# Optimization experiments

Hardware: AMD Instinct MI355X
Metric: run time of the kernel (lower is better)

The kernel has to match this reference:

```python
import jax, jax.numpy as jnp
import numpy as np

RADIUS = 0.2
NSAMPLE = 32
NPOINT = 2048
EPS = 1e-5


def setup_inputs() -> dict:
    key = jax.random.key(0)
    ks = jax.random.split(key, 6)
    B, N, C = 8, 8192, 64
    xyz = jax.random.uniform(ks[0], (B, N, 3), dtype=jnp.float32)
    features = jax.random.normal(ks[1], (B, C, N), dtype=jnp.float32)
    W1 = jax.random.normal(ks[2], (64, 67), dtype=jnp.float32) * 0.1
    W2 = jax.random.normal(ks[3], (64, 64), dtype=jnp.float32) * 0.1
    W3 = jax.random.normal(ks[4], (128, 64), dtype=jnp.float32) * 0.1
    return {
        'xyz': xyz, 'features': features,
        'W1': W1, 'g1': jnp.ones((64,), jnp.float32), 'b1': jnp.zeros((64,), jnp.float32),
        'W2': W2, 'g2': jnp.ones((64,), jnp.float32), 'b2': jnp.zeros((64,), jnp.float32),
        'W3': W3, 'g3': jnp.ones((128,), jnp.float32), 'b3': jnp.zeros((128,), jnp.float32),
    }


def furthest_point_sample(xyz, npoint):
    # xyz: (B, N, 3) -> (B, npoint) int32 indices, first index is 0 (CUDA FPS convention)
    B, N, _ = xyz.shape
    idxs0 = jnp.zeros((B, npoint), dtype=jnp.int32)
    dists0 = jnp.full((B, N), 1e10, dtype=xyz.dtype)
    last0 = jnp.zeros((B,), dtype=jnp.int32)

    def body(i, state):
        idxs, dists, last = state
        last_pt = xyz[jnp.arange(B), last]                      # (B, 3)
        d = jnp.sum((xyz - last_pt[:, None, :]) ** 2, axis=-1)  # (B, N)
        dists = jnp.minimum(dists, d)
        nxt = jnp.argmax(dists, axis=-1).astype(jnp.int32)
        idxs = idxs.at[:, i].set(nxt)
        return (idxs, dists, nxt)

    idxs, _, _ = jax.lax.fori_loop(1, npoint, body, (idxs0, dists0, last0))
    return idxs


def ball_query(xyz, new_xyz, radius, nsample):
    # Returns (B, S, nsample) int32: first `nsample` points within radius of each
    # query center, padded with the first in-ball index (pointnet2 convention).
    N = xyz.shape[1]
    d2 = jnp.sum((new_xyz[:, :, None, :] - xyz[:, None, :, :]) ** 2, axis=-1)  # (B,S,N)
    key = jnp.where(d2 < radius * radius, jnp.arange(N, dtype=jnp.int32), N)
    neg_vals, _ = jax.lax.top_k(-key, nsample)   # k smallest keys = earliest in-ball indices
    cand = -neg_vals                             # (B, S, nsample)
    first = cand[..., :1]
    return jnp.where(cand < N, cand, first)


def reference(xyz, features, W1, g1, b1, W2, g2, b2, W3, g3, b3):
    B = xyz.shape[0]
    fps_idx = furthest_point_sample(xyz, NPOINT)              # (B, S)
    new_xyz = xyz[jnp.arange(B)[:, None], fps_idx]            # (B, S, 3)

    idx = ball_query(xyz, new_xyz, RADIUS, NSAMPLE)           # (B, S, ns)
    bb = jnp.arange(B)[:, None, None]
    grouped_xyz = xyz[bb, idx] - new_xyz[:, :, None, :]       # (B, S, ns, 3) relative coords
    grouped_f = features.transpose(0, 2, 1)[bb, idx]          # (B, S, ns, C)
    g = jnp.concatenate([grouped_xyz, grouped_f], axis=-1)    # (B, S, ns, 3+C)
    g = g.transpose(0, 3, 1, 2)                               # (B, 3+C, S, ns)

    for W, ga, be in ((W1, g1, b1), (W2, g2, b2), (W3, g3, b3)):
        h = jnp.einsum('oc,bcsn->bosn', W, g)                 # 1x1 conv
        mu = h.mean(axis=(0, 2, 3), keepdims=True)            # training-mode BN stats
        var = h.var(axis=(0, 2, 3), keepdims=True)
        h = (h - mu) / jnp.sqrt(var + EPS)
        g = jax.nn.relu(h * ga[None, :, None, None] + be[None, :, None, None])

    feats = g.max(axis=-1)                                    # (B, mlp[-1], S)
    return new_xyz, feats
```

## Files before the change

kernel.cpp:

```cpp
#include <hip/hip_runtime.h>
#include <hip/hip_bf16.h>
#include <stdint.h>

#define NB 8
#define NN 8192
#define NC 64
#define NS 2048
#define NK 32
#define NCOL (NB*NS*NK)

typedef float v2f __attribute__((ext_vector_type(2)));

__device__ __forceinline__ unsigned short f2bf(float x) {
    union { float f; unsigned u; } c; c.f = x;
    unsigned r = c.u + 0x7fffu + ((c.u >> 16) & 1u);
    return (unsigned short)(r >> 16);
}
__device__ __forceinline__ float bf2f(unsigned v16) {
    union { float f; unsigned u; } c; c.u = v16 << 16;
    return c.f;
}

template<int CTRL>
__device__ __forceinline__ unsigned long long dpp_max_u64(unsigned long long key) {
    int olo = __builtin_amdgcn_update_dpp(0, (int)(unsigned)key,        CTRL, 0xf, 0xf, true);
    int ohi = __builtin_amdgcn_update_dpp(0, (int)(unsigned)(key >> 32), CTRL, 0xf, 0xf, true);
    unsigned long long ok = ((unsigned long long)(unsigned)ohi << 32) | (unsigned)olo;
    return ok > key ? ok : key;
}
template<int CTRL>
__device__ __forceinline__ float dpp_add_f32(float x) {
    int o = __builtin_amdgcn_update_dpp(0, __float_as_int(x), CTRL, 0xf, 0xf, true);
    return x + __int_as_float(o);
}
template<int CTRL>
__device__ __forceinline__ float dpp_max_f32(float x) {
    int o = __builtin_amdgcn_update_dpp(__float_as_int(x), __float_as_int(x), CTRL, 0xf, 0xf, false);
    return fmaxf(x, __int_as_float(o));
}
template<int CTRL>
__device__ __forceinline__ float dpp_min_f32(float x) {
    int o = __builtin_amdgcn_update_dpp(__float_as_int(x), __float_as_int(x), CTRL, 0xf, 0xf, false);
    return fminf(x, __int_as_float(o));
}
template<int CTRL, int RM>
__device__ __forceinline__ unsigned dpp_add_u32(unsigned x) {
    int o = __builtin_amdgcn_update_dpp(0, (int)x, CTRL, RM, 0xf, true);
    return x + (unsigned)o;
}
__device__ __forceinline__ float wave_red_min(float x) {
    x = dpp_min_f32<0x111>(x); x = dpp_min_f32<0x112>(x);
    x = dpp_min_f32<0x114>(x); x = dpp_min_f32<0x118>(x);
    x = dpp_min_f32<0x142>(x); x = dpp_min_f32<0x143>(x);
    return __int_as_float(__builtin_amdgcn_readlane(__float_as_int(x), 63));
}
__device__ __forceinline__ float wave_red_max(float x) {
    x = dpp_max_f32<0x111>(x); x = dpp_max_f32<0x112>(x);
    x = dpp_max_f32<0x114>(x); x = dpp_max_f32<0x118>(x);
    x = dpp_max_f32<0x142>(x); x = dpp_max_f32<0x143>(x);
    return __int_as_float(__builtin_amdgcn_readlane(__float_as_int(x), 63));
}
__device__ __forceinline__ v2f relu2(v2f v) {
    v.x = fmaxf(v.x, 0.f); v.y = fmaxf(v.y, 0.f); return v;
}

__device__ __forceinline__ unsigned expand_bits10(unsigned v) {
    v = (v * 0x00010001u) & 0xFF0000FFu;
    v = (v * 0x00000101u) & 0x0F00F00Fu;
    v = (v * 0x00000011u) & 0xC30C30C3u;
    v = (v * 0x00000005u) & 0x49249249u;
    return v;
}
__global__ __launch_bounds__(1024) void sort_kernel(const float* __restrict__ xyz,
    float4* __restrict__ sorted)
{
    __shared__ unsigned cnt[2048];
    __shared__ unsigned codes[NN];
    __shared__ unsigned wsum[16];
    const int b = blockIdx.x;
    const int tid = threadIdx.x;
    const int w = tid >> 6;
    const int lane = tid & 63;
    const float* xb = xyz + (size_t)b * NN * 3;
    cnt[tid] = 0; cnt[tid + 1024] = 0;
    __syncthreads();
    for (int p = tid; p < NN; p += 1024) {
        float x = xb[3*p+0], y = xb[3*p+1], z = xb[3*p+2];
        int qx = (int)(x * 1024.f); qx = qx < 0 ? 0 : (qx > 1023 ? 1023 : qx);
        int qy = (int)(y * 1024.f); qy = qy < 0 ? 0 : (qy > 1023 ? 1023 : qy);
        int qz = (int)(z * 1024.f); qz = qz < 0 ? 0 : (qz > 1023 ? 1023 : qz);
        unsigned m = expand_bits10((unsigned)qx)
                   | (expand_bits10((unsigned)qy) << 1)
                   | (expand_bits10((unsigned)qz) << 2);
        unsigned bk = m >> 19;
        codes[p] = bk;
        atomicAdd(&cnt[bk], 1u);
    }
    __syncthreads();
    unsigned c0 = cnt[2*tid], c1 = cnt[2*tid+1];
    unsigned s = c0 + c1;
    unsigned v = s;
    v = dpp_add_u32<0x111, 0xf>(v);
    v = dpp_add_u32<0x112, 0xf>(v);
    v = dpp_add_u32<0x114, 0xf>(v);
    v = dpp_add_u32<0x118, 0xf>(v);
    v = dpp_add_u32<0x142, 0xa>(v);
    v = dpp_add_u32<0x143, 0xc>(v);
    if (lane == 63) wsum[w] = v;
    __syncthreads();
    unsigned wbase = 0;
#pragma unroll
    for (int j = 0; j < 15; ++j) {
        unsigned t = wsum[j];
        wbase += (j < w) ? t : 0u;
    }
    unsigned excl = wbase + v - s;
    cnt[2*tid]   = excl;
    cnt[2*tid+1] = excl + c0;
    __syncthreads();
    for (int p = tid; p < NN; p += 1024) {
        unsigned bk = codes[p];
        unsigned pos = atomicAdd(&cnt[bk], 1u);
        float4 o;
        o.x = xb[3*p+0]; o.y = xb[3*p+1]; o.z = xb[3*p+2];
        o.w = __int_as_float(p);
        sorted[(size_t)b * NN + pos] = o;
    }
}

__global__ __launch_bounds__(1024) void fps_kernel(const float* __restrict__ xyz,
    const float4* __restrict__ sorted,
    float* __restrict__ new_xyz, float* __restrict__ out_newxyz)
{
#pragma clang fp contract(off)
    const int b = blockIdx.x;
    const int tid = threadIdx.x;
    const int w = tid >> 6;
    const int lane = tid & 63;
    __shared__ float sx[NN], sy[NN], sz[NN];
    __shared__ float s_hist[NS * 3];
    __shared__ unsigned long long s_slot[3];
    const float4* sp = sorted + (size_t)b * NN + (size_t)w * 512 + lane;
    v2f px[4], py[4], pz[4], dmin[4];
    unsigned plo[8];
    float bnx = 1e30f, bny = 1e30f, bnz = 1e30f;
    float bxx = -1e30f, bxy = -1e30f, bxz = -1e30f;
#pragma unroll
    for (int m = 0; m < 4; ++m) {
        float4 a = sp[128*m];
        float4 c = sp[128*m + 64];
        px[m].x = a.x; px[m].y = c.x;
        py[m].x = a.y; py[m].y = c.y;
        pz[m].x = a.z; pz[m].y = c.z;
        dmin[m].x = 1e10f; dmin[m].y = 1e10f;
        int ia = __float_as_int(a.w), ic = __float_as_int(c.w);
        plo[2*m]   = ~(unsigned)ia;
        plo[2*m+1] = ~(unsigned)ic;
        sx[ia] = a.x; sy[ia] = a.y; sz[ia] = a.z;
        sx[ic] = c.x; sy[ic] = c.y; sz[ic] = c.z;
        bnx = fminf(bnx, fminf(a.x, c.x)); bxx = fmaxf(bxx, fmaxf(a.x, c.x));
        bny = fminf(bny, fminf(a.y, c.y)); bxy = fmaxf(bxy, fmaxf(a.y, c.y));
        bnz = fminf(bnz, fminf(a.z, c.z)); bxz = fmaxf(bxz, fmaxf(a.z, c.z));
    }
    bnx = wave_red_min(bnx); bny = wave_red_min(bny); bnz = wave_red_min(bnz);
    bxx = wave_red_max(bxx); bxy = wave_red_max(bxy); bxz = wave_red_max(bxz);

    const float* xb = xyz + (size_t)b * NN * 3;
    float lx = xb[0], ly = xb[1], lz = xb[2];
    if (tid == 0) {
        s_hist[0] = lx; s_hist[1] = ly; s_hist[2] = lz;
        s_slot[0] = 0ull; s_slot[1] = 0ull; s_slot[2] = 0ull;
    }
    float ckv = 1e30f;
    unsigned cklo = 0u;
    __syncthreads();

    int cur = 1, nxt = 2;
    for (int i = 1; i < NS; ++i) {
        if (tid == 0) s_slot[nxt] = 0ull;
        float cdx = fmaxf(fmaxf(bnx - lx, lx - bxx), 0.f);
        float cdy = fmaxf(fmaxf(bny - ly, ly - bxy), 0.f);
        float cdz = fmaxf(fmaxf(bnz - lz, lz - bxz), 0.f);
        float lb = (cdx*cdx + cdy*cdy) + cdz*cdz;
        if (!(lb >= ckv)) {
            v2f l2x; l2x.x = lx; l2x.y = lx;
            v2f l2y; l2y.x = ly; l2y.y = ly;
            v2f l2z; l2z.x = lz; l2z.y = lz;
            unsigned long long best = 0ull;
#pragma unroll
            for (int m = 0; m < 4; ++m) {
                v2f dx = px[m] - l2x;
                v2f dy = py[m] - l2y;
                v2f dz = pz[m] - l2z;
                v2f d = (dx*dx + dy*dy) + dz*dz;
                v2f dm;
                dm.x = fminf(dmin[m].x, d.x);
                dm.y = fminf(dmin[m].y, d.y);
                dmin[m] = dm;
                unsigned long long k0 =
                    ((unsigned long long)__float_as_uint(dm.x) << 32) | plo[2*m];
                unsigned long long k1 =
                    ((unsigned long long)__float_as_uint(dm.y) << 32) | plo[2*m+1];
                if (k0 > best) best = k0;
                if (k1 > best) best = k1;
            }
            best = dpp_max_u64<0x111>(best);
            best = dpp_max_u64<0x112>(best);
            best = dpp_max_u64<0x114>(best);
            best = dpp_max_u64<0x118>(best);
            best = dpp_max_u64<0x142>(best);
            best = dpp_max_u64<0x143>(best);
            ckv  = __uint_as_float((unsigned)__builtin_amdgcn_readlane((int)(best >> 32), 63));
            cklo = (unsigned)__builtin_amdgcn_readlane((int)(best & 0xffffffffull), 63);
        }
        if (lane == 0)
            atomicMax(&s_slot[cur],
                      ((unsigned long long)__float_as_uint(ckv) << 32) | cklo);
        __syncthreads();
        const unsigned long long k = s_slot[cur];
        const int ix = ~(int)(unsigned)(k & 0xffffffffull);
        lx = sx[ix]; ly = sy[ix]; lz = sz[ix];
        if (tid == 0) {
            s_hist[3*i+0] = lx; s_hist[3*i+1] = ly; s_hist[3*i+2] = lz;
        }
        cur = nxt;
        nxt = nxt + 1; if (nxt == 3) nxt = 0;
    }
    __syncthreads();
    float* nw = new_xyz + (size_t)b * NS * 3;
    float* ow = out_newxyz + (size_t)b * NS * 3;
    for (int t = tid; t < NS * 3; t += 1024) {
        float v = s_hist[t];
        nw[t] = v; ow[t] = v;
    }
}

__global__ __launch_bounds__(256) void transpose_kernel(const float* __restrict__ f,
    float* __restrict__ ft)
{
    __shared__ float tile[64][65];
    int b = blockIdx.y;
    int p0 = blockIdx.x * 64;
    for (int k = threadIdx.x; k < 64*64; k += 256) {
        int c = k >> 6, p = k & 63;
        tile[c][p] = f[((size_t)b * NC + c) * NN + p0 + p];
    }
    __syncthreads();
    for (int k = threadIdx.x; k < 64*64; k += 256) {
        int p = k >> 6, c = k & 63;
        ft[((size_t)b * NN + p0 + p) * NC + c] = tile[c][p];
    }
}

__global__ __launch_bounds__(256) void ballquery_kernel(const float* __restrict__ xyz,
    const float* __restrict__ new_xyz, int* __restrict__ idx)
{
#pragma clang fp contract(off)
    const int q = blockIdx.x * 4 + (threadIdx.x >> 6);
    const int lane = threadIdx.x & 63;
    const int b = q >> 11;
    const float r2 = (float)(0.2 * 0.2);
    const float* xb = xyz + (size_t)b * NN * 3;
    const float* nx = new_xyz + (size_t)q * 3;
    float qx = nx[0], qy = nx[1], qz = nx[2];
    int cnt = 0, first = -1;
    int* out = idx + (size_t)q * NK;
    for (int base = 0; base < NN; base += 64) {
        int p = base + lane;
        float x = xb[p*3+0], y = xb[p*3+1], z = xb[p*3+2];
        float dx = qx - x, dy = qy - y, dz = qz - z;
        float d2 = (dx*dx + dy*dy) + dz*dz;
        bool in = d2 < r2;
        unsigned long long m = __ballot(in);
        if (m) {
            if (first < 0) first = base + __builtin_ctzll(m);
            if (in) {
                int rank = cnt + __popcll(m & ((1ull << lane) - 1ull));
                if (rank < NK) out[rank] = p;
            }
            cnt += __popcll(m);
            if (cnt >= NK) break;
        }
    }
    for (int k = cnt + lane; k < NK; k += 64) out[k] = first;
}

__global__ __launch_bounds__(256, 2) void layer1_kernel(const float* __restrict__ xyz,
    const float* __restrict__ new_xyz, const int* __restrict__ idx,
    const float* __restrict__ ft, const float* __restrict__ W1,
    unsigned short* __restrict__ h1)
{
    const int col = blockIdx.x * 256 + threadIdx.x;
    const int b = col >> 16;
    const int s = (col >> 5) & 2047;
    const int p = idx[col];
    v2f g[34];
    float* gf = (float*)g;
    {
        const float* nx = new_xyz + ((size_t)(b * NS + s)) * 3;
        const float* xp = xyz + ((size_t)(b * NN + p)) * 3;
        gf[0] = xp[0] - nx[0]; gf[1] = xp[1] - nx[1]; gf[2] = xp[2] - nx[2];
    }
    const float4* fp = (const float4*)(ft + ((size_t)(b * NN + p)) * NC);
#pragma unroll
    for (int c4 = 0; c4 < 16; ++c4) {
        float4 v = fp[c4];
        gf[3 + 4*c4 + 0] = v.x; gf[3 + 4*c4 + 1] = v.y;
        gf[3 + 4*c4 + 2] = v.z; gf[3 + 4*c4 + 3] = v.w;
    }
    gf[67] = 0.f;
    uint4* dst = (uint4*)(h1 + (size_t)col * 64);
#pragma unroll
    for (int half = 0; half < 2; ++half) {
        float h[32];
#pragma unroll 4
        for (int o16 = 0; o16 < 32; ++o16) {
            const float* w = W1 + (half*32 + o16) * 67;
            v2f acc; acc.x = 0.f; acc.y = 0.f;
#pragma unroll
            for (int k = 0; k < 33; ++k) {
                v2f wv; wv.x = w[2*k]; wv.y = w[2*k+1];
                acc = wv * g[k] + acc;
            }
            h[o16] = fmaf(w[66], gf[66], acc.x + acc.y);
        }
#pragma unroll
        for (int k = 0; k < 4; ++k) {
            uint4 v;
            v.x = (unsigned)f2bf(h[8*k+0]) | ((unsigned)f2bf(h[8*k+1]) << 16);
            v.y = (unsigned)f2bf(h[8*k+2]) | ((unsigned)f2bf(h[8*k+3]) << 16);
            v.z = (unsigned)f2bf(h[8*k+4]) | ((unsigned)f2bf(h[8*k+5]) << 16);
            v.w = (unsigned)f2bf(h[8*k+6]) | ((unsigned)f2bf(h[8*k+7]) << 16);
            dst[half*4 + k] = v;
        }
    }
}

__global__ __launch_bounds__(256) void stats_kernel(const unsigned short* __restrict__ h,
    float* __restrict__ sums)
{
    __shared__ float ls[64], lq[64];
    const int tid = threadIdx.x;
    if (tid < 64) { ls[tid] = 0.f; lq[tid] = 0.f; }
    __syncthreads();
    float s[8] = {0,0,0,0,0,0,0,0}, q[8] = {0,0,0,0,0,0,0,0};
    const int gt = blockIdx.x * 256 + tid;
    const int G = gridDim.x * 256;
    const uint4* src = (const uint4*)h;
    const int nvec = NCOL * 8;
    for (int i = gt; i < nvec; i += G) {
        uint4 v = src[i];
        float f0 = bf2f(v.x & 0xffffu), f1 = bf2f(v.x >> 16);
        float f2 = bf2f(v.y & 0xffffu), f3 = bf2f(v.y >> 16);
        float f4 = bf2f(v.z & 0xffffu), f5 = bf2f(v.z >> 16);
        float f6 = bf2f(v.w & 0xffffu), f7 = bf2f(v.w >> 16);
        s[0] += f0; q[0] = fmaf(f0, f0, q[0]);
        s[1] += f1; q[1] = fmaf(f1, f1, q[1]);
        s[2] += f2; q[2] = fmaf(f2, f2, q[2]);
        s[3] += f3; q[3] = fmaf(f3, f3, q[3]);
        s[4] += f4; q[4] = fmaf(f4, f4, q[4]);
        s[5] += f5; q[5] = fmaf(f5, f5, q[5]);
        s[6] += f6; q[6] = fmaf(f6, f6, q[6]);
        s[7] += f7; q[7] = fmaf(f7, f7, q[7]);
    }
    const int obase = (tid & 7) * 8;
#pragma unroll
    for (int j = 0; j < 8; ++j) {
        atomicAdd(&ls[obase + j], s[j]);
        atomicAdd(&lq[obase + j], q[j]);
    }
    __syncthreads();
    if (tid < 64) {
        atomicAdd(&sums[tid*2+0], ls[tid]);
        atomicAdd(&sums[tid*2+1], lq[tid]);
    }
}

__global__ void finalize_kernel(const float* __restrict__ sums,
    const float* __restrict__ gamma, const float* __restrict__ beta,
    float* __restrict__ ab, int nch)
{
    int c = threadIdx.x;
    if (c < nch) {
        const float invM = 1.0f / 524288.0f;
        float mu = sums[c*2] * invM;
        float var = sums[c*2+1] * invM - mu * mu;
        float a = gamma[c] / sqrtf(var + 1e-5f);
        ab[c] = a;
        ab[nch + c] = fmaf(-mu, a, beta[c]);
    }
}

__global__ __launch_bounds__(256, 2) void layer2_kernel(const unsigned short* __restrict__ h1,
    const float* __restrict__ ab1, const float* __restrict__ W2,
    unsigned short* __restrict__ h2)
{
    const int col = blockIdx.x * 256 + threadIdx.x;
    const uint4* src = (const uint4*)(h1 + (size_t)col * 64);
    v2f g[32];
    float* gf = (float*)g;
#pragma unroll
    for (int k = 0; k < 8; ++k) {
        uint4 v = src[k];
        gf[8*k+0] = bf2f(v.x & 0xffffu); gf[8*k+1] = bf2f(v.x >> 16);
        gf[8*k+2] = bf2f(v.y & 0xffffu); gf[8*k+3] = bf2f(v.y >> 16);
        gf[8*k+4] = bf2f(v.z & 0xffffu); gf[8*k+5] = bf2f(v.z >> 16);
        gf[8*k+6] = bf2f(v.w & 0xffffu); gf[8*k+7] = bf2f(v.w >> 16);
    }
    const v2f* a2 = (const v2f*)ab1;
    const v2f* b2 = (const v2f*)(ab1 + 64);
#pragma unroll
    for (int k = 0; k < 32; ++k)
        g[k] = relu2(a2[k] * g[k] + b2[k]);
    uint4* dst = (uint4*)(h2 + (size_t)col * 64);
#pragma unroll
    for (int half = 0; half < 2; ++half) {
        float h[32];
#pragma unroll 4
        for (int o16 = 0; o16 < 32; ++o16) {
            const float* w = W2 + ((half*32 + o16) << 6);
            v2f acc; acc.x = 0.f; acc.y = 0.f;
#pragma unroll
            for (int k = 0; k < 32; ++k) {
                v2f wv; wv.x = w[2*k]; wv.y = w[2*k+1];
                acc = wv * g[k] + acc;
            }
            h[o16] = acc.x + acc.y;
        }
#pragma unroll
        for (int k = 0; k < 4; ++k) {
            uint4 v;
            v.x = (unsigned)f2bf(h[8*k+0]) | ((unsigned)f2bf(h[8*k+1]) << 16);
            v.y = (unsigned)f2bf(h[8*k+2]) | ((unsigned)f2bf(h[8*k+3]) << 16);
            v.z = (unsigned)f2bf(h[8*k+4]) | ((unsigned)f2bf(h[8*k+5]) << 16);
            v.w = (unsigned)f2bf(h[8*k+6]) | ((unsigned)f2bf(h[8*k+7]) << 16);
            dst[half*4 + k] = v;
        }
    }
}

__global__ __launch_bounds__(256, 2) void layer3_kernel(const unsigned short* __restrict__ h2,
    const float* __restrict__ ab2, const float* __restrict__ W3,
    float* __restrict__ hmax, float* __restrict__ hmin, float* __restrict__ sums3)
{
    __shared__ float ls[128], lq[128];
    const int tid = threadIdx.x;
    if (tid < 128) { ls[tid] = 0.f; lq[tid] = 0.f; }
    __syncthreads();
    const int col = blockIdx.x * 256 + tid;
    const int q = col >> 5;
    const uint4* src = (const uint4*)(h2 + (size_t)col * 64);
    v2f g[32];
    float* gf = (float*)g;
#pragma unroll
    for (int k = 0; k < 8; ++k) {
        uint4 v = src[k];
        gf[8*k+0] = bf2f(v.x & 0xffffu); gf[8*k+1] = bf2f(v.x >> 16);
        gf[8*k+2] = bf2f(v.y & 0xffffu); gf[8*k+3] = bf2f(v.y >> 16);
        gf[8*k+4] = bf2f(v.z & 0xffffu); gf[8*k+5] = bf2f(v.z >> 16);
        gf[8*k+6] = bf2f(v.w & 0xffffu); gf[8*k+7] = bf2f(v.w >> 16);
    }
    const v2f* a2 = (const v2f*)ab2;
    const v2f* b2 = (const v2f*)(ab2 + 64);
#pragma unroll
    for (int k = 0; k < 32; ++k)
        g[k] = relu2(a2[k] * g[k] + b2[k]);
    const bool leader = ((tid & 31) == 31);
#pragma unroll 2
    for (int o = 0; o < 128; ++o) {
        const float* w = W3 + (o << 6);
        v2f acc; acc.x = 0.f; acc.y = 0.f;
#pragma unroll
        for (int k = 0; k < 32; ++k) {
            v2f wv; wv.x = w[2*k]; wv.y = w[2*k+1];
            acc = wv * g[k] + acc;
        }
        float hv = acc.x + acc.y;
        float sm = hv, sq = hv*hv, mx = hv, mn = hv;
        sm = dpp_add_f32<0x111>(sm); sq = dpp_add_f32<0x111>(sq);
        mx = dpp_max_f32<0x111>(mx); mn = dpp_min_f32<0x111>(mn);
        sm = dpp_add_f32<0x112>(sm); sq = dpp_add_f32<0x112>(sq);
        mx = dpp_max_f32<0x112>(mx); mn = dpp_min_f32<0x112>(mn);
        sm = dpp_add_f32<0x114>(sm); sq = dpp_add_f32<0x114>(sq);
        mx = dpp_max_f32<0x114>(mx); mn = dpp_min_f32<0x114>(mn);
        sm = dpp_add_f32<0x118>(sm); sq = dpp_add_f32<0x118>(sq);
        mx = dpp_max_f32<0x118>(mx); mn = dpp_min_f32<0x118>(mn);
        sm = dpp_add_f32<0x142>(sm); sq = dpp_add_f32<0x142>(sq);
        mx = dpp_max_f32<0x142>(mx); mn = dpp_min_f32<0x142>(mn);
        if (leader) {
            hmax[(size_t)o * 16384 + q] = mx;
            hmin[(size_t)o * 16384 + q] = mn;
            atomicAdd(&ls[o], sm);
            atomicAdd(&lq[o], sq);
        }
    }
    __syncthreads();
    if (tid < 128) {
        atomicAdd(&sums3[tid*2+0], ls[tid]);
        atomicAdd(&sums3[tid*2+1], lq[tid]);
    }
}

__global__ __launch_bounds__(256) void final_kernel(const float* __restrict__ hmax,
    const float* __restrict__ hmin, const float* __restrict__ ab3,
    float* __restrict__ out)
{
    const int t = blockIdx.x * 256 + threadIdx.x;
    const int s = t & 2047;
    const int o = (t >> 11) & 127;
    const int b = t >> 18;
    const int q = (b << 11) + s;
    float a = ab3[o], c = ab3[128 + o];
    float h = (a >= 0.f) ? hmax[(size_t)o * 16384 + q] : hmin[(size_t)o * 16384 + q];
    out[t] = fmaxf(fmaf(a, h, c), 0.f);
}

extern "C" void kernel_launch(void* const* d_in, const int* in_sizes, int n_in,
                              void* d_out, int out_size, void* d_ws, size_t ws_size,
                              hipStream_t stream) {
    (void)in_sizes; (void)n_in; (void)out_size; (void)ws_size;
    const float* xyz      = (const float*)d_in[0];
    const float* features = (const float*)d_in[1];
    const float* W1 = (const float*)d_in[2];
    const float* g1 = (const float*)d_in[3];
    const float* b1 = (const float*)d_in[4];
    const float* W2 = (const float*)d_in[5];
    const float* g2 = (const float*)d_in[6];
    const float* b2 = (const float*)d_in[7];
    const float* W3 = (const float*)d_in[8];
    const float* g3 = (const float*)d_in[9];
    const float* b3 = (const float*)d_in[10];

    char* ws = (char*)d_ws;
    float*          new_xyz = (float*)(ws + 0);
    int*            idx     = (int*)(ws + 196608);
    float*          ft      = (float*)(ws + 2293760);
    unsigned short* h1      = (unsigned short*)(ws + 19070976);
    unsigned short* h2      = (unsigned short*)(ws + 86179840);
    float*          hmax    = (float*)(ws + 153288704);
    float*          hmin    = (float*)(ws + 161677312);
    float*          sums    = (float*)(ws + 170065920);
    float*          ab      = (float*)(ws + 170067968);
    float* sums1 = sums;        float* ab1 = ab;
    float* sums2 = sums + 128;  float* ab2 = ab + 128;
    float* sums3 = sums + 256;  float* ab3 = ab + 256;

    float4* sorted = (float4*)h1;

    float* out_newxyz = (float*)d_out;
    float* out_feats  = (float*)d_out + 49152;

    hipMemsetAsync(sums, 0, 2048, stream);

    sort_kernel<<<NB, 1024, 0, stream>>>(xyz, sorted);
    fps_kernel<<<NB, 1024, 0, stream>>>(xyz, sorted, new_xyz, out_newxyz);
    transpose_kernel<<<dim3(NN/64, NB), 256, 0, stream>>>(features, ft);
    ballquery_kernel<<<(NB*NS)/4, 256, 0, stream>>>(xyz, new_xyz, idx);
    layer1_kernel<<<NCOL/256, 256, 0, stream>>>(xyz, new_xyz, idx, ft, W1, h1);
    stats_kernel<<<1024, 256, 0, stream>>>(h1, sums1);
    finalize_kernel<<<1, 128, 0, stream>>>(sums1, g1, b1, ab1, 64);
    layer2_kernel<<<NCOL/256, 256, 0, stream>>>(h1, ab1, W2, h2);
    stats_kernel<<<1024, 256, 0, stream>>>(h2, sums2);
    finalize_kernel<<<1, 128, 0, stream>>>(sums2, g2, b2, ab2, 64);
    layer3_kernel<<<NCOL/256, 256, 0, stream>>>(h2, ab2, W3, hmax, hmin, sums3);
    finalize_kernel<<<1, 128, 0, stream>>>(sums3, g3, b3, ab3, 128);
    final_kernel<<<(NB*128*NS)/256, 256, 0, stream>>>(hmax, hmin, ab3, out_feats);
}
```

Baseline: 2.039 ms.

## Use bf16 MFMA for layer-3 conv and simplify FPS atomic key

Rewrites the layer-3 1x1 convolution to use 16x16x32 bf16 MFMA instructions instead of per-thread scalar FMAs. Each wave now handles two 32-sample groups, applies the BN2 affine and ReLU while packing activations into bf16 fragments, and keeps per-channel sums and sums of squares in registers, reducing them once at the end. Max and min are reduced with DPP across the 16 columns. The weights are now rounded to bf16, which lowers precision, and W3 is re-converted on every tile. In FPS, lane 63 submits the full 64-bit key directly, dropping one readlane per iteration.

```diff
diff --git a/kernel.cpp b/kernel.cpp
--- a/kernel.cpp
+++ b/kernel.cpp
@@ -10,6 +10,8 @@
 #define NCOL (NB*NS*NK)
 
 typedef float v2f __attribute__((ext_vector_type(2)));
+typedef __attribute__((ext_vector_type(8))) short bf16x8;
+typedef __attribute__((ext_vector_type(4))) float f32x4;
 
 __device__ __forceinline__ unsigned short f2bf(float x) {
     union { float f; unsigned u; } c; c.f = x;
@@ -172,7 +174,7 @@
         s_slot[0] = 0ull; s_slot[1] = 0ull; s_slot[2] = 0ull;
     }
     float ckv = 1e30f;
-    unsigned cklo = 0u;
+    unsigned long long kc = 0ull;
     __syncthreads();
 
     int cur = 1, nxt = 2;
@@ -210,12 +212,11 @@
             best = dpp_max_u64<0x118>(best);
             best = dpp_max_u64<0x142>(best);
             best = dpp_max_u64<0x143>(best);
-            ckv  = __uint_as_float((unsigned)__builtin_amdgcn_readlane((int)(best >> 32), 63));
-            cklo = (unsigned)__builtin_amdgcn_readlane((int)(best & 0xffffffffull), 63);
-        }
-        if (lane == 0)
-            atomicMax(&s_slot[cur],
-                      ((unsigned long long)__float_as_uint(ckv) << 32) | cklo);
+            kc = best;
+            ckv = __uint_as_float((unsigned)__builtin_amdgcn_readlane((int)(best >> 32), 63));
+        }
+        if (lane == 63)
+            atomicMax(&s_slot[cur], kc);
         __syncthreads();
         const unsigned long long k = s_slot[cur];
         const int ix = ~(int)(unsigned)(k & 0xffffffffull);
@@ -447,49 +448,86 @@
     const int tid = threadIdx.x;
     if (tid < 128) { ls[tid] = 0.f; lq[tid] = 0.f; }
     __syncthreads();
-    const int col = blockIdx.x * 256 + tid;
-    const int q = col >> 5;
-    const uint4* src = (const uint4*)(h2 + (size_t)col * 64);
-    v2f g[32];
-    float* gf = (float*)g;
-#pragma unroll
-    for (int k = 0; k < 8; ++k) {
-        uint4 v = src[k];
-        gf[8*k+0] = bf2f(v.x & 0xffffu); gf[8*k+1] = bf2f(v.x >> 16);
-        gf[8*k+2] = bf2f(v.y & 0xffffu); gf[8*k+3] = bf2f(v.y >> 16);
-        gf[8*k+4] = bf2f(v.z & 0xffffu); gf[8*k+5] = bf2f(v.z >> 16);
-        gf[8*k+6] = bf2f(v.w & 0xffffu); gf[8*k+7] = bf2f(v.w >> 16);
-    }
-    const v2f* a2 = (const v2f*)ab2;
-    const v2f* b2 = (const v2f*)(ab2 + 64);
-#pragma unroll
-    for (int k = 0; k < 32; ++k)
-        g[k] = relu2(a2[k] * g[k] + b2[k]);
-    const bool leader = ((tid & 31) == 31);
-#pragma unroll 2
-    for (int o = 0; o < 128; ++o) {
-        const float* w = W3 + (o << 6);
-        v2f acc; acc.x = 0.f; acc.y = 0.f;
-#pragma unroll
-        for (int k = 0; k < 32; ++k) {
-            v2f wv; wv.x = w[2*k]; wv.y = w[2*k+1];
-            acc = wv * g[k] + acc;
-        }
-        float hv = acc.x + acc.y;
-        float sm = hv, sq = hv*hv, mx = hv, mn = hv;
+    const int lane = tid & 63;
+    const int col0 = lane & 15;
+    const int rg   = lane >> 4;
+    const int wglob = blockIdx.x * 4 + (tid >> 6);
+
+    float sums[32], sqs[32];
+#pragma unroll
+    for (int t = 0; t < 32; ++t) { sums[t] = 0.f; sqs[t] = 0.f; }
+
+    for (int g = wglob * 2; g < wglob * 2 + 2; ++g) {
+        bf16x8 Bf[2][2];
+#pragma unroll
+        for (int t = 0; t < 2; ++t) {
+            const int col = g * 32 + t * 16 + col0;
+            const unsigned short* hp = h2 + (size_t)col * 64 + rg * 8;
+#pragma unroll
+            for (int kh = 0; kh < 2; ++kh) {
+                uint4 hv = *(const uint4*)(hp + kh * 32);
+                const float* ap = ab2 + kh * 32 + rg * 8;
+                float4 a0 = *(const float4*)ap;
+                float4 a1 = *(const float4*)(ap + 4);
+                float4 b0 = *(const float4*)(ap + 64);
+                float4 b1 = *(const float4*)(ap + 68);
+                bf16x8 f;
+                f[0] = (short)f2bf(fmaxf(fmaf(a0.x, bf2f(hv.x & 0xffffu), b0.x), 0.f));
+                f[1] = (short)f2bf(fmaxf(fmaf(a0.y, bf2f(hv.x >> 16),     b0.y), 0.f));
+                f[2] = (short)f2bf(fmaxf(fmaf(a0.z, bf2f(hv.y & 0xffffu), b0.z), 0.f));
+                f[3] = (short)f2bf(fmaxf(fmaf(a0.w, bf2f(hv.y >> 16),     b0.w), 0.f));
+                f[4] = (short)f2bf(fmaxf(fmaf(a1.x, bf2f(hv.z & 0xffffu), b1.x), 0.f));
+                f[5] = (short)f2bf(fmaxf(fmaf(a1.y, bf2f(hv.z >> 16),     b1.y), 0.f));
+                f[6] = (short)f2bf(fmaxf(fmaf(a1.z, bf2f(hv.w & 0xffffu), b1.z), 0.f));
+                f[7] = (short)f2bf(fmaxf(fmaf(a1.w, bf2f(hv.w >> 16),     b1.w), 0.f));
+                Bf[t][kh] = f;
+            }
+        }
+#pragma unroll
+        for (int rt = 0; rt < 8; ++rt) {
+            f32x4 acc0 = {0.f, 0.f, 0.f, 0.f};
+            f32x4 acc1 = {0.f, 0.f, 0.f, 0.f};
+#pragma unroll
+            for (int kh = 0; kh < 2; ++kh) {
+                const float* wp = W3 + (size_t)(rt * 16 + col0) * 64 + kh * 32 + rg * 8;
+                float4 w0 = *(const float4*)wp;
+                float4 w1 = *(const float4*)(wp + 4);
+                bf16x8 Af;
+                Af[0] = (short)f2bf(w0.x); Af[1] = (short)f2bf(w0.y);
+                Af[2] = (short)f2bf(w0.z); Af[3] = (short)f2bf(w0.w);
+                Af[4] = (short)f2bf(w1.x); Af[5] = (short)f2bf(w1.y);
+                Af[6] = (short)f2bf(w1.z); Af[7] = (short)f2bf(w1.w);
+                acc0 = __builtin_amdgcn_mfma_f32_16x16x32_bf16(Af, Bf[0][kh], acc0, 0, 0, 0);
+                acc1 = __builtin_amdgcn_mfma_f32_16x16x32_bf16(Af, Bf[1][kh], acc1, 0, 0, 0);
+            }
+#pragma unroll
+            for (int r = 0; r < 4; ++r) {
+                float v0 = acc0[r], v1 = acc1[r];
+                sums[rt*4 + r] += v0 + v1;
+                sqs[rt*4 + r]  = fmaf(v0, v0, fmaf(v1, v1, sqs[rt*4 + r]));
+                float mx = fmaxf(v0, v1);
+                float mn = fminf(v0, v1);
+                mx = dpp_max_f32<0x111>(mx); mn = dpp_min_f32<0x111>(mn);
+                mx = dpp_max_f32<0x112>(mx); mn = dpp_min_f32<0x112>(mn);
+                mx = dpp_max_f32<0x114>(mx); mn = dpp_min_f32<0x114>(mn);
+                mx = dpp_max_f32<0x118>(mx); mn = dpp_min_f32<0x118>(mn);
+                if (col0 == 15) {
+                    const int o = rt * 16 + rg * 4 + r;
+                    hmax[(size_t)o * 16384 + g] = mx;
+                    hmin[(size_t)o * 16384 + g] = mn;
+                }
+            }
+        }
+    }
+#pragma unroll
+    for (int t = 0; t < 32; ++t) {
+        float sm = sums[t], sq = sqs[t];
         sm = dpp_add_f32<0x111>(sm); sq = dpp_add_f32<0x111>(sq);
-        mx = dpp_max_f32<0x111>(mx); mn = dpp_min_f32<0x111>(mn);
         sm = dpp_add_f32<0x112>(sm); sq = dpp_add_f32<0x112>(sq);
-        mx = dpp_max_f32<0x112>(mx); mn = dpp_min_f32<0x112>(mn);
         sm = dpp_add_f32<0x114>(sm); sq = dpp_add_f32<0x114>(sq);
-        mx = dpp_max_f32<0x114>(mx); mn = dpp_min_f32<0x114>(mn);
         sm = dpp_add_f32<0x118>(sm); sq = dpp_add_f32<0x118>(sq);
-        mx = dpp_max_f32<0x118>(mx); mn = dpp_min_f32<0x118>(mn);
-        sm = dpp_add_f32<0x142>(sm); sq = dpp_add_f32<0x142>(sq);
-        mx = dpp_max_f32<0x142>(mx); mn = dpp_min_f32<0x142>(mn);
-        if (leader) {
-            hmax[(size_t)o * 16384 + q] = mx;
-            hmin[(size_t)o * 16384 + q] = mn;
+        if (col0 == 15) {
+            const int o = (t >> 2) * 16 + rg * 4 + (t & 3);
             atomicAdd(&ls[o], sm);
             atomicAdd(&lq[o], sq);
         }
```

After: 2.029 ms. No clear change (-0.5%).
